# Kernel tuning notes

Hardware: AMD Instinct MI355X
Metric: run time of the kernel (lower is better)

Reference implementation:

```python
import jax, jax.numpy as jnp
import numpy as np

N = 50000
D = 256
K = 16  # fixed neighbor-list degree (regularized form of the ragged edge_dict)


def setup_inputs() -> dict:
    key = jax.random.key(0)
    k1, k2, k3, k4 = jax.random.split(key, 4)
    feats = jax.random.normal(k1, (N, D), dtype=jnp.float32)
    edge_dict = jax.random.randint(k2, (N, K), 0, N)  # int32 neighbor indices
    W = jax.random.normal(k3, (D, D), dtype=jnp.float32) * (1.0 / np.sqrt(D))
    b = jax.random.normal(k4, (D,), dtype=jnp.float32) * 0.01
    idx = jnp.arange(N)
    sadj = jnp.zeros((1,), dtype=jnp.float32)
    epoch = 0
    return {"idx": idx, "feats": feats, "edge_dict": edge_dict,
            "sadj": sadj, "epoch": epoch, "W": W, "b": b}


def reference(idx, feats, edge_dict, sadj, epoch, W, b):
    # fc -> relu (dropout is identity in eval mode; p=0.5 train-only)
    x = jax.nn.relu(feats @ W.T + b)  # [N, D]
    # region_aggregate: per-node mean over fixed-degree neighbor lists
    pooled = jnp.mean(x[edge_dict], axis=1)  # gather [N, K, D] -> mean -> [N, D]
    return pooled
```

## Files before the change

kernel.cpp:

```cpp
#include <hip/hip_runtime.h>
#include <hip/hip_bf16.h>

#define NN  50000
#define DD  256
#define KNB 16
#define BM  64
#define NSL 8
#define SLW 32
#define NKT 8
#define NGRP ((NN + 63) / 64)

typedef __attribute__((ext_vector_type(8))) short bf16x8;
typedef __attribute__((ext_vector_type(4))) float f32x4;
typedef __attribute__((ext_vector_type(4))) int   i32x4;

static __device__ __forceinline__ float bf2f(unsigned int u16) {
    union { unsigned int i; float f; } c; c.i = u16 << 16; return c.f;
}
static __device__ __forceinline__ float bf2f_hi(unsigned int u) {
    union { unsigned int i; float f; } c; c.i = u & 0xffff0000u; return c.f;
}
static __device__ __forceinline__ short f2bf(float f) {
    union { float f; unsigned int i; } c; c.f = f;
    unsigned int r = c.i + 0x7FFFu + ((c.i >> 16) & 1u);
    return (short)(r >> 16);
}
static __device__ __forceinline__ bf16x8 pack8(float4 a, float4 b) {
    union { __hip_bfloat162 h[4]; bf16x8 v; } u;
    u.h[0] = __float22bfloat162_rn(make_float2(a.x, a.y));
    u.h[1] = __float22bfloat162_rn(make_float2(a.z, a.w));
    u.h[2] = __float22bfloat162_rn(make_float2(b.x, b.y));
    u.h[3] = __float22bfloat162_rn(make_float2(b.z, b.w));
    return u.v;
}

#define GLOAD_LDS16(g, l) \
    __builtin_amdgcn_global_load_lds((const __attribute__((address_space(1))) unsigned int*)(g), \
                                     (__attribute__((address_space(3))) unsigned int*)(l), 16, 0, 0)

__global__ void convert_w(const float* __restrict__ W, unsigned short* __restrict__ Wbf)
{
    int s = blockIdx.x * blockDim.x + threadIdx.x;
    if (s >= 8192) return;
    int j  = s & 15;
    int kb = (s >> 4) & 3;
    int nb = (s >> 6) & 15;
    int kt = s >> 10;
    const float4* p = (const float4*)(W + (nb * 16 + j) * DD + kt * 32 + kb * 8);
    *(bf16x8*)&Wbf[(size_t)s * 8] = pack8(p[0], p[1]);
}

__global__ __launch_bounds__(256, 2) void gemm_relu(
    const float* __restrict__ feats, const unsigned short* __restrict__ Wbf,
    const float* __restrict__ bias, unsigned short* __restrict__ xs)
{
    __shared__ short At[16384];
    __shared__ short Wt[2][8192];

    const int tid  = threadIdx.x;
    const int lane = tid & 63;
    const int wc   = tid >> 6;
    const int l15  = lane & 15;
    const int lg   = lane >> 4;
    const int blockRow = blockIdx.x * BM;

    auto wstage = [&](int kt, int buf) {
        const char* src = (const char*)Wbf + kt * 16384 + tid * 16;
        char* dst = (char*)&Wt[buf][0] + tid * 16;
        #pragma unroll
        for (int c = 0; c < 4; ++c)
            GLOAD_LDS16(src + c * 4096, dst + c * 4096);
    };

    wstage(0, 0);
    {
        const int r = tid >> 2, q = tid & 3;
        int row = blockRow + r; if (row > NN - 1) row = NN - 1;
        const float* base = feats + (size_t)row * DD;
        const int m = r >> 4, i15 = r & 15;
        #pragma unroll
        for (int h = 0; h < 4; ++h) {
            float4 v[4];
            #pragma unroll
            for (int j = 0; j < 4; ++j)
                v[j] = *(const float4*)(base + h * 64 + j * 16 + q * 4);
            #pragma unroll
            for (int j = 0; j < 4; ++j) {
                int k0 = h * 64 + j * 16 + q * 4;
                int kt = k0 >> 5, kq = (k0 >> 3) & 3, eo = k0 & 7;
                union { __hip_bfloat162 h2[2]; uint2 u; } p;
                p.h2[0] = __float22bfloat162_rn(make_float2(v[j].x, v[j].y));
                p.h2[1] = __float22bfloat162_rn(make_float2(v[j].z, v[j].w));
                int el = (((kt * 4 + m) * 4 + kq) * 16 + i15) * 8 + eo;
                *(uint2*)&At[el] = p.u;
            }
        }
    }

    float bv[4];
    #pragma unroll
    for (int n = 0; n < 4; ++n) bv[n] = bias[wc * 64 + n * 16 + l15];

    f32x4 acc[4][4];
    #pragma unroll
    for (int m = 0; m < 4; ++m)
        #pragma unroll
        for (int n = 0; n < 4; ++n) acc[m][n] = (f32x4)0.0f;

    __syncthreads();

    #pragma unroll
    for (int kt = 0; kt < NKT; ++kt) {
        const int cur = kt & 1;
        if (kt + 1 < NKT) wstage(kt + 1, cur ^ 1);

        bf16x8 afr[4], bfr[4];
        #pragma unroll
        for (int m = 0; m < 4; ++m)
            afr[m] = *(const bf16x8*)&At[(((kt * 4 + m) * 4 + lg) * 16 + l15) * 8];
        #pragma unroll
        for (int n = 0; n < 4; ++n)
            bfr[n] = *(const bf16x8*)&Wt[cur][(((wc * 4 + n) * 4 + lg) * 16 + l15) * 8];

        #pragma unroll
        for (int m = 0; m < 4; ++m)
            #pragma unroll
            for (int n = 0; n < 4; ++n)
                acc[m][n] = __builtin_amdgcn_mfma_f32_16x16x32_bf16(
                    afr[m], bfr[n], acc[m][n], 0, 0, 0);

        __syncthreads();
    }

    #pragma unroll
    for (int n = 0; n < 4; ++n) {
        const int sl = wc * 2 + (n >> 1);
        const int c  = (n & 1) * 16 + l15;
        unsigned short* xb = xs + (size_t)sl * NN * SLW + c;
        #pragma unroll
        for (int m = 0; m < 4; ++m) {
            int rbase = blockRow + m * 16 + (lg << 2);
            f32x4 a = acc[m][n];
            #pragma unroll
            for (int r = 0; r < 4; ++r) {
                int row = rbase + r;
                if (row < NN) {
                    float vv = fmaxf(a[r] + bv[n], 0.0f);
                    xb[(size_t)row * SLW] = (unsigned short)f2bf(vv);
                }
            }
        }
    }
}

__global__ __launch_bounds__(256) void gather_mean(
    const int* __restrict__ edge, const unsigned short* __restrict__ xs,
    float* __restrict__ out)
{
    const int s    = blockIdx.x & 7;
    const int lane = threadIdx.x & 63;
    const int w    = threadIdx.x >> 6;
    const int g    = lane >> 2, q = lane & 3;
    const unsigned short* xsl = xs + (size_t)s * NN * SLW;
    const unsigned qo = q * 8;

    for (int grp = blockIdx.x >> 3; grp < NGRP; grp += 256) {
        const int iw0 = grp * 64 + w * 16;
        const int i   = iw0 + g;

        int eoff = iw0 * KNB + lane * 4;
        if (eoff > NN * KNB - 4) eoff = NN * KNB - 4;
        i32x4 e4 = *(const i32x4*)(edge + eoff);
        int e[4] = { e4[0], e4[1], e4[2], e4[3] };

        float a[8];
        #pragma unroll
        for (int j = 0; j < 8; ++j) a[j] = 0.0f;

        #pragma unroll
        for (int k = 0; k < KNB; ++k) {
            int src = (lane & 60) | (k >> 2);
            unsigned n = (unsigned)__shfl(e[k & 3], src, 64);
            bf16x8 v = *(const bf16x8*)(xsl + n * SLW + qo);
            const unsigned int* vu = (const unsigned int*)&v;
            #pragma unroll
            for (int j = 0; j < 4; ++j) {
                a[2 * j]     += bf2f(vu[j] & 0xffffu);
                a[2 * j + 1] += bf2f_hi(vu[j]);
            }
        }

        if (i < NN) {
            f32x4 o0 = { a[0] * 0.0625f, a[1] * 0.0625f, a[2] * 0.0625f, a[3] * 0.0625f };
            f32x4 o1 = { a[4] * 0.0625f, a[5] * 0.0625f, a[6] * 0.0625f, a[7] * 0.0625f };
            float* op = out + (size_t)i * DD + s * SLW + q * 8;
            __builtin_nontemporal_store(o0, (f32x4*)op);
            __builtin_nontemporal_store(o1, (f32x4*)(op + 4));
        }
    }
}

extern "C" void kernel_launch(void* const* d_in, const int* in_sizes, int n_in,
                              void* d_out, int out_size, void* d_ws, size_t ws_size,
                              hipStream_t stream) {
    const float* feats = (const float*)d_in[1];
    const int*   edge  = (const int*)d_in[2];
    const float* W     = (const float*)d_in[5];
    const float* b     = (const float*)d_in[6];
    float* out = (float*)d_out;

    unsigned short* xs  = (unsigned short*)d_ws;
    unsigned short* Wbf = (unsigned short*)((char*)d_ws + (size_t)NN * DD * 2);

    convert_w<<<dim3(32), dim3(256), 0, stream>>>(W, Wbf);
    gemm_relu<<<dim3(NGRP), dim3(256), 0, stream>>>(feats, Wbf, b, xs);
    gather_mean<<<dim3(2048), dim3(256), 0, stream>>>(edge, xs, out);
}
```

Baseline: 66.53 us.

## Split GEMM columns across two blocks, load A directly to registers, batch gather loads

The GEMM now launches two blocks per 64-row tile, each computing 128 output columns. Each block preloads its whole half of W into LDS once, so the per-k-tile double-buffered staging and the barriers inside the loop go away. A fragments are read straight from global fp32 and packed to bf16 in registers instead of being staged through LDS, which means each feats row is read twice, once per column block. The gather kernel now issues eight neighbor loads before accumulating them, to keep more memory requests in flight.

```diff
diff --git a/kernel.cpp b/kernel.cpp
--- a/kernel.cpp
+++ b/kernel.cpp
@@ -54,89 +54,72 @@
     const float* __restrict__ feats, const unsigned short* __restrict__ Wbf,
     const float* __restrict__ bias, unsigned short* __restrict__ xs)
 {
-    __shared__ short At[16384];
-    __shared__ short Wt[2][8192];
+    __shared__ short Wt[32768];
 
     const int tid  = threadIdx.x;
     const int lane = tid & 63;
     const int wc   = tid >> 6;
     const int l15  = lane & 15;
     const int lg   = lane >> 4;
-    const int blockRow = blockIdx.x * BM;
-
-    auto wstage = [&](int kt, int buf) {
-        const char* src = (const char*)Wbf + kt * 16384 + tid * 16;
-        char* dst = (char*)&Wt[buf][0] + tid * 16;
-        #pragma unroll
-        for (int c = 0; c < 4; ++c)
-            GLOAD_LDS16(src + c * 4096, dst + c * 4096);
-    };
-
-    wstage(0, 0);
+    const int rg   = blockIdx.x >> 1;
+    const int cg   = blockIdx.x & 1;
+    const int blockRow = rg * BM;
+
     {
-        const int r = tid >> 2, q = tid & 3;
-        int row = blockRow + r; if (row > NN - 1) row = NN - 1;
-        const float* base = feats + (size_t)row * DD;
-        const int m = r >> 4, i15 = r & 15;
-        #pragma unroll
-        for (int h = 0; h < 4; ++h) {
-            float4 v[4];
-            #pragma unroll
-            for (int j = 0; j < 4; ++j)
-                v[j] = *(const float4*)(base + h * 64 + j * 16 + q * 4);
-            #pragma unroll
-            for (int j = 0; j < 4; ++j) {
-                int k0 = h * 64 + j * 16 + q * 4;
-                int kt = k0 >> 5, kq = (k0 >> 3) & 3, eo = k0 & 7;
-                union { __hip_bfloat162 h2[2]; uint2 u; } p;
-                p.h2[0] = __float22bfloat162_rn(make_float2(v[j].x, v[j].y));
-                p.h2[1] = __float22bfloat162_rn(make_float2(v[j].z, v[j].w));
-                int el = (((kt * 4 + m) * 4 + kq) * 16 + i15) * 8 + eo;
-                *(uint2*)&At[el] = p.u;
-            }
-        }
-    }
-
-    float bv[4];
-    #pragma unroll
-    for (int n = 0; n < 4; ++n) bv[n] = bias[wc * 64 + n * 16 + l15];
-
-    f32x4 acc[4][4];
+        const char* wsrc = (const char*)Wbf + cg * 8192 + tid * 16;
+        char* wdst = (char*)Wt + tid * 16;
+        #pragma unroll
+        for (int p = 0; p < 16; ++p)
+            GLOAD_LDS16(wsrc + (p >> 1) * 16384 + (p & 1) * 4096,
+                        wdst + p * 4096);
+    }
+
+    const float* aptr[4];
+    #pragma unroll
+    for (int m = 0; m < 4; ++m) {
+        int r = blockRow + m * 16 + l15;
+        if (r > NN - 1) r = NN - 1;
+        aptr[m] = feats + (size_t)r * DD + lg * 8;
+    }
+
+    float bv[2];
+    #pragma unroll
+    for (int n = 0; n < 2; ++n) bv[n] = bias[cg * 128 + wc * 32 + n * 16 + l15];
+
+    f32x4 acc[4][2];
     #pragma unroll
     for (int m = 0; m < 4; ++m)
         #pragma unroll
-        for (int n = 0; n < 4; ++n) acc[m][n] = (f32x4)0.0f;
+        for (int n = 0; n < 2; ++n) acc[m][n] = (f32x4)0.0f;
 
     __syncthreads();
 
     #pragma unroll
     for (int kt = 0; kt < NKT; ++kt) {
-        const int cur = kt & 1;
-        if (kt + 1 < NKT) wstage(kt + 1, cur ^ 1);
-
-        bf16x8 afr[4], bfr[4];
+        bf16x8 afr[4], bfr[2];
+        #pragma unroll
+        for (int m = 0; m < 4; ++m) {
+            float4 lo = *(const float4*)(aptr[m] + kt * 32);
+            float4 hi = *(const float4*)(aptr[m] + kt * 32 + 4);
+            afr[m] = pack8(lo, hi);
+        }
+        #pragma unroll
+        for (int n = 0; n < 2; ++n)
+            bfr[n] = *(const bf16x8*)&Wt[(((kt * 8 + wc * 2 + n) * 4 + lg) * 16 + l15) * 8];
+
         #pragma unroll
         for (int m = 0; m < 4; ++m)
-            afr[m] = *(const bf16x8*)&At[(((kt * 4 + m) * 4 + lg) * 16 + l15) * 8];
-        #pragma unroll
-        for (int n = 0; n < 4; ++n)
-            bfr[n] = *(const bf16x8*)&Wt[cur][(((wc * 4 + n) * 4 + lg) * 16 + l15) * 8];
-
-        #pragma unroll
-        for (int m = 0; m < 4; ++m)
-            #pragma unroll
-            for (int n = 0; n < 4; ++n)
+            #pragma unroll
+            for (int n = 0; n < 2; ++n)
                 acc[m][n] = __builtin_amdgcn_mfma_f32_16x16x32_bf16(
                     afr[m], bfr[n], acc[m][n], 0, 0, 0);
-
-        __syncthreads();
-    }
-
-    #pragma unroll
-    for (int n = 0; n < 4; ++n) {
-        const int sl = wc * 2 + (n >> 1);
-        const int c  = (n & 1) * 16 + l15;
-        unsigned short* xb = xs + (size_t)sl * NN * SLW + c;
+    }
+
+    const int sl = cg * 4 + wc;
+    unsigned short* xbase = xs + (size_t)sl * NN * SLW;
+    #pragma unroll
+    for (int n = 0; n < 2; ++n) {
+        const int c = n * 16 + l15;
         #pragma unroll
         for (int m = 0; m < 4; ++m) {
             int rbase = blockRow + m * 16 + (lg << 2);
@@ -146,7 +129,7 @@
                 int row = rbase + r;
                 if (row < NN) {
                     float vv = fmaxf(a[r] + bv[n], 0.0f);
-                    xb[(size_t)row * SLW] = (unsigned short)f2bf(vv);
+                    xbase[(size_t)row * SLW + c] = (unsigned short)f2bf(vv);
                 }
             }
         }
@@ -178,15 +161,23 @@
         for (int j = 0; j < 8; ++j) a[j] = 0.0f;
 
         #pragma unroll
-        for (int k = 0; k < KNB; ++k) {
-            int src = (lane & 60) | (k >> 2);
-            unsigned n = (unsigned)__shfl(e[k & 3], src, 64);
-            bf16x8 v = *(const bf16x8*)(xsl + n * SLW + qo);
-            const unsigned int* vu = (const unsigned int*)&v;
-            #pragma unroll
-            for (int j = 0; j < 4; ++j) {
-                a[2 * j]     += bf2f(vu[j] & 0xffffu);
-                a[2 * j + 1] += bf2f_hi(vu[j]);
+        for (int half = 0; half < 2; ++half) {
+            bf16x8 vbuf[8];
+            #pragma unroll
+            for (int kk = 0; kk < 8; ++kk) {
+                int k = half * 8 + kk;
+                int src = (lane & 60) | (k >> 2);
+                unsigned n = (unsigned)__shfl(e[k & 3], src, 64);
+                vbuf[kk] = *(const bf16x8*)(xsl + n * SLW + qo);
+            }
+            #pragma unroll
+            for (int kk = 0; kk < 8; ++kk) {
+                const unsigned int* vu = (const unsigned int*)&vbuf[kk];
+                #pragma unroll
+                for (int j = 0; j < 4; ++j) {
+                    a[2 * j]     += bf2f(vu[j] & 0xffffu);
+                    a[2 * j + 1] += bf2f_hi(vu[j]);
+                }
             }
         }
 
@@ -213,6 +204,6 @@
     unsigned short* Wbf = (unsigned short*)((char*)d_ws + (size_t)NN * DD * 2);
 
     convert_w<<<dim3(32), dim3(256), 0, stream>>>(W, Wbf);
-    gemm_relu<<<dim3(NGRP), dim3(256), 0, stream>>>(feats, Wbf, b, xs);
+    gemm_relu<<<dim3(NGRP * 2), dim3(256), 0, stream>>>(feats, Wbf, b, xs);
     gather_mean<<<dim3(2048), dim3(256), 0, stream>>>(edge, xs, out);
 }
```

New measurement: 101.3 us. 1.52x slower.
